# Kernel optimization log

Measured on AMD Instinct MI355X. Metric: run time of the kernel, lower is better.

Reference implementation:

```python
import jax, jax.numpy as jnp
import numpy as np
from jax import lax

NMS_TH = 0.05
TOPK_P = 1000
NMS_IOU = 0.5
NUMDETS = 100
NMS_ITERS = 15
IM = 2048.0
SIZES = [256, 128, 64, 32, 16]
NUM_CLASS = 80


def _make_boxes(key, n):
    k1, k2, k3, k4 = jax.random.split(key, 4)
    cy = jax.random.uniform(k1, (n,)) * IM
    cx = jax.random.uniform(k2, (n,)) * IM
    h = jax.random.uniform(k3, (n,)) * 300.0 + 16.0
    w = jax.random.uniform(k4, (n,)) * 300.0 + 16.0
    # yxyx boxes
    return jnp.stack([cy - h / 2, cx - w / 2, cy + h / 2, cx + w / 2], axis=1)


def setup_inputs() -> dict:
    key = jax.random.key(0)
    inp = {}
    for s, sz in enumerate(SIZES):
        kc = jax.random.fold_in(key, 2 * s)
        kb = jax.random.fold_in(key, 2 * s + 1)
        n = sz * sz
        inp['cls%d' % s] = jax.random.normal(kc, (1, n, NUM_CLASS), jnp.float32) - 2.0
        inp['reg%d' % s] = _make_boxes(kb, n)[None]
    inp['locations'] = jnp.array([0.0, 0.0, IM - 1.0, IM - 1.0, 1024.0, 1024.0], jnp.float32)
    return inp


def _pairwise_iou(a, b):
    # a: (N,4) yxyx, b: (M,4) yxyx -> (N,M)
    area_a = jnp.clip(a[:, 2] - a[:, 0], 0) * jnp.clip(a[:, 3] - a[:, 1], 0)
    area_b = jnp.clip(b[:, 2] - b[:, 0], 0) * jnp.clip(b[:, 3] - b[:, 1], 0)
    iy1 = jnp.maximum(a[:, None, 0], b[None, :, 0])
    ix1 = jnp.maximum(a[:, None, 1], b[None, :, 1])
    iy2 = jnp.minimum(a[:, None, 2], b[None, :, 2])
    ix2 = jnp.minimum(a[:, None, 3], b[None, :, 3])
    inter = jnp.clip(iy2 - iy1, 0) * jnp.clip(ix2 - ix1, 0)
    union = area_a[:, None] + area_b[None, :] - inter
    return inter / jnp.maximum(union, 1e-9)


def _cluster_nms(boxes, scores, classes, valid, iou_th):
    order = jnp.argsort(-scores)
    b = boxes[order]
    s = scores[order]
    c = classes[order]
    v = valid[order]
    iou = jnp.triu(_pairwise_iou(b, b), k=1)  # (K,K)

    def body(B, _):
        max_a = B.max(axis=0)
        keep_col = (max_a <= iou_th).astype(B.dtype)[:, None]
        return iou * keep_col, None

    B, _ = lax.scan(body, iou, None, length=NMS_ITERS)
    keep = (B.max(axis=0) <= iou_th) & v
    return b, s, c, keep


def _per_level(cls_s, reg_s):
    p = jax.nn.sigmoid(cls_s[0])                 # (N, C)
    ps = p.max(axis=1)                           # (N,)
    pi = p.argmax(axis=1).astype(jnp.int32) + 1  # class index, 0 is background
    m = ps > NMS_TH
    ps_m = jnp.where(m, ps, -1.0)
    k = min(TOPK_P, ps_m.shape[0])
    top_s, top_idx = lax.top_k(ps_m, k)
    return top_s, pi[top_idx], reg_s[0][top_idx], m[top_idx]


def reference(cls0, cls1, cls2, cls3, cls4, reg0, reg1, reg2, reg3, reg4, locations):
    levels = [(cls0, reg0), (cls1, reg1), (cls2, reg2), (cls3, reg3), (cls4, reg4)]
    sc, cl, bx, vd = [], [], [], []
    for cls_s, reg_s in levels:
        s_, c_, b_, v_ = _per_level(cls_s, reg_s)
        sc.append(s_); cl.append(c_); bx.append(b_); vd.append(v_)
    scores = jnp.concatenate(sc)
    classes = jnp.concatenate(cl)
    boxes = jnp.concatenate(bx, axis=0)
    valid = jnp.concatenate(vd)
    scores = jnp.where(valid, scores, 0.0)

    vy1, vx1, vy2, vx2 = locations[0], locations[1], locations[2], locations[3]
    ori_h, ori_w = locations[4], locations[5]
    boxes = jnp.stack([
        jnp.maximum(boxes[:, 0], vy1), jnp.maximum(boxes[:, 1], vx1),
        jnp.minimum(boxes[:, 2], vy2), jnp.minimum(boxes[:, 3], vx2)], axis=1)

    b, s, c, keep = _cluster_nms(boxes, scores, classes, valid, NMS_IOU)
    s = jnp.where(keep, s, 0.0)
    top_s, sel = lax.top_k(s, NUMDETS)
    bbox = b[sel]
    cls_out = c[sel]

    # transfer boxes back to original-image coordinates
    sy = ori_h / jnp.maximum(vy2 - vy1, 1e-6)
    sx = ori_w / jnp.maximum(vx2 - vx1, 1e-6)
    bbox = jnp.stack([
        (bbox[:, 0] - vy1) * sy, (bbox[:, 1] - vx1) * sx,
        (bbox[:, 2] - vy1) * sy, (bbox[:, 3] - vx1) * sx], axis=1)
    return bbox, cls_out, top_s
```

## Files before the change

kernel.cpp:

```cpp
#include <hip/hip_runtime.h>
#include <math.h>

#define NANCH 87296
#define NF 4256
#define CAPD 128
#define NITER 16
#define BCAP 512
#define EC 8192
#define NBLK 341
#define BASE20 0xBD4CCu
#define NB20 9216
#define BPT 9

struct InPtrs {
    const float* cls[5];
    const float* reg[5];
    const float* loc;
};

constexpr size_t SZ_HIST  = 5ull * NB20 * 4;
constexpr size_t OFF_HIST = 0;
constexpr size_t OFF_CNT  = OFF_HIST + SZ_HIST;
constexpr size_t OFF_CTR  = OFF_CNT + (size_t)NF * 4;
constexpr size_t ZERO_SZ  = OFF_CTR + 64;
constexpr size_t OFF_SBITS = ((ZERO_SZ + 255) / 256) * 256;
constexpr size_t OFF_CLSV  = OFF_SBITS + (size_t)NANCH * 4;
constexpr size_t OFF_PAR   = OFF_CLSV + (size_t)NANCH * 4;
constexpr size_t OFF_INVB  = OFF_PAR + 128;
constexpr size_t OFF_INVO  = OFF_INVB + (size_t)NBLK * 4;
constexpr size_t OFF_FINK  = ((OFF_INVO + (size_t)NBLK * 4 + 255) / 256) * 256;
constexpr size_t OFF_BBUF  = OFF_FINK + (size_t)NF * 8;
constexpr size_t OFF_SBOX  = OFF_BBUF + 5ull * BCAP * 8;
constexpr size_t OFF_SSC   = OFF_SBOX + (size_t)NF * 16;
constexpr size_t OFF_SCV   = OFF_SSC + (size_t)NF * 4;
constexpr size_t OFF_SAR   = OFF_SCV + (size_t)NF * 4;
constexpr size_t OFF_NBR   = OFF_SAR + (size_t)NF * 4;

__device__ __forceinline__ void lvl_of(int a, int& lev, int& idx) {
    if (a < 65536)      { lev = 0; idx = a; }
    else if (a < 81920) { lev = 1; idx = a - 65536; }
    else if (a < 86016) { lev = 2; idx = a - 81920; }
    else if (a < 87040) { lev = 3; idx = a - 86016; }
    else                { lev = 4; idx = a - 87040; }
}

__device__ __forceinline__ unsigned int fkey(float f) {
    unsigned int u = __float_as_uint(f);
    return u ^ ((u & 0x80000000u) ? 0xFFFFFFFFu : 0x80000000u);
}
__device__ __forceinline__ float funkey(unsigned int k) {
    return __uint_as_float(k ^ ((k & 0x80000000u) ? 0x80000000u : 0xFFFFFFFFu));
}
__device__ __forceinline__ unsigned int bin20_addr(unsigned int v) {
    unsigned int owner = v / BPT;
    unsigned int i = v - owner * BPT;
    return (i << 10) | owner;
}

__global__ __launch_bounds__(1024) void k1_score(InPtrs P, unsigned int* hist,
        unsigned int* sbits, unsigned int* clsv, unsigned int* invBlk) {
    int t = threadIdx.x;
    int a = blockIdx.x * 256 + (t >> 2);
    int k = t & 3;
    int lev, idx; lvl_of(a, lev, idx);
    const float4* row = (const float4*)(P.cls[lev] + (size_t)idx * 80);
    float4 v[5];
    #pragma unroll
    for (int q = 0; q < 5; ++q) v[q] = row[q * 4 + k];
    float best = -INFINITY; int bi = 0;
    #pragma unroll
    for (int q = 0; q < 5; ++q) {
        int c0 = q * 16 + k * 4;
        if (v[q].x > best) { best = v[q].x; bi = c0 + 0; }
        if (v[q].y > best) { best = v[q].y; bi = c0 + 1; }
        if (v[q].z > best) { best = v[q].z; bi = c0 + 2; }
        if (v[q].w > best) { best = v[q].w; bi = c0 + 3; }
    }
    #pragma unroll
    for (int m = 1; m < 4; m <<= 1) {
        float ob = __shfl_xor(best, m, 64);
        int  obi = __shfl_xor(bi, m, 64);
        if (ob > best || (ob == best && obi < bi)) { best = ob; bi = obi; }
    }
    bool lead = (k == 0);
    unsigned int valid = 0;
    if (lead) {
        float score = 1.0f / (1.0f + expf(-best));
        valid = (score > 0.05f) ? 1u : 0u;
        float psm = valid ? score : -1.0f;
        unsigned int sb = fkey(psm);
        sbits[a] = sb;
        clsv[a] = (unsigned int)(bi + 1) | (valid << 31);
        if (valid) {
            unsigned int bin = (sb >> 12) - BASE20;
            atomicAdd(&hist[(size_t)lev * NB20 + bin20_addr(bin)], 1u);
        }
    }
    __shared__ unsigned int wv[16];
    unsigned long long mv = __ballot(lead && valid);
    int lane = t & 63, w = t >> 6;
    if (lane == 0) wv[w] = (unsigned int)__popcll(mv);
    __syncthreads();
    if (t == 0) {
        unsigned int s = 0;
        #pragma unroll
        for (int i = 0; i < 16; ++i) s += wv[i];
        invBlk[blockIdx.x] = 256u - s;
    }
}

__global__ __launch_bounds__(1024) void k2_scan(const unsigned int* hist,
        const unsigned int* invBlk, unsigned int* params, unsigned int* invOff) {
    int t = threadIdx.x;
    if (blockIdx.x == 5) {
        __shared__ unsigned int sv[512];
        __shared__ unsigned int orig[512];
        if (t < 512) {
            unsigned int v = (t < NBLK) ? invBlk[t] : 0u;
            sv[t] = v; orig[t] = v;
        }
        __syncthreads();
        for (int off = 1; off < 512; off <<= 1) {
            unsigned int add = 0;
            if (t < 512 && t >= off) add = sv[t - off];
            __syncthreads();
            if (t < 512) sv[t] += add;
            __syncthreads();
        }
        if (t < NBLK) {
            int segStart = (t < 256) ? 0 : (t < 320) ? 256 : (t < 336) ? 320
                         : (t < 340) ? 336 : 340;
            invOff[t] = sv[t] - orig[t] - (segStart > 0 ? sv[segStart - 1] : 0u);
        }
        return;
    }
    int lev = blockIdx.x;
    unsigned int K = (lev == 4) ? 256u : 1000u;
    const unsigned int* h = hist + (size_t)lev * NB20;
    __shared__ unsigned int seg[1024];
    __shared__ unsigned int suf[1024];
    unsigned int hc[BPT];
    unsigned int s = 0;
    #pragma unroll
    for (int i = 0; i < BPT; ++i) { hc[i] = h[(i << 10) | t]; s += hc[i]; }
    seg[t] = s;
    suf[t] = s;
    __syncthreads();
    for (int off = 1; off < 1024; off <<= 1) {
        unsigned int v = suf[t];
        unsigned int add = (t + off < 1024) ? suf[t + off] : 0u;
        __syncthreads();
        suf[t] = v + add;
        __syncthreads();
    }
    unsigned int totValid = suf[0];
    if (totValid >= K) {
        unsigned int excl = suf[t] - seg[t];
        if (excl < K && excl + seg[t] >= K) {
            unsigned int cum = excl;
            for (int i = BPT - 1; i >= 0; --i) {
                unsigned int c = hc[i];
                if (cum + c >= K) {
                    params[lev] = (unsigned int)(t * BPT + i);
                    params[8 + lev] = K - cum;
                    params[16 + lev] = 0;
                    break;
                }
                cum += c;
            }
        }
    } else if (t == 0) {
        params[lev] = 0;
        params[8 + lev] = 0;
        params[16 + lev] = K - totValid;
    }
}

__global__ __launch_bounds__(256) void k3_compact(const unsigned int* sbits,
        const unsigned int* clsv, const unsigned int* params,
        const unsigned int* invOff, unsigned long long* finKeys,
        unsigned int* ctrs, unsigned long long* bBuf) {
    int blk = blockIdx.x;
    int t = threadIdx.x;
    int a = blk * 256 + t;
    int lev, idx; lvl_of(a, lev, idx);
    unsigned int sb = sbits[a];
    unsigned int cv = clsv[a];
    unsigned int bin = (sb >> 12) - BASE20;
    unsigned int Bs = params[lev];
    unsigned int rNeg = params[16 + lev];
    unsigned int valid = cv >> 31;
    int lane = t & 63, w = t >> 6;
    unsigned long long lt = (1ull << lane) - 1ull;
    __shared__ unsigned int wInv[4], wFin[4], wB[4];
    __shared__ unsigned int baseFin, baseB;
    unsigned long long mInv = __ballot(valid == 0u);
    if (lane == 0) wInv[w] = (unsigned int)__popcll(mInv);
    __syncthreads();
    unsigned int invRank = invOff[blk] + (unsigned int)__popcll(mInv & lt);
    for (int i = 0; i < w; ++i) invRank += wInv[i];
    bool isFin, isB;
    if (valid) {
        isFin = (bin > Bs);
        isB   = (bin == Bs);
    } else {
        isFin = (rNeg > 0) && (invRank < rNeg);
        isB   = false;
    }
    unsigned long long mFin = __ballot(isFin);
    unsigned long long mB   = __ballot(isB);
    if (lane == 0) { wFin[w] = (unsigned int)__popcll(mFin); wB[w] = (unsigned int)__popcll(mB); }
    __syncthreads();
    if (t == 0) {
        unsigned int tf = wFin[0] + wFin[1] + wFin[2] + wFin[3];
        unsigned int tb = wB[0] + wB[1] + wB[2] + wB[3];
        baseFin = tf ? atomicAdd(&ctrs[0], tf) : 0u;
        baseB   = tb ? atomicAdd(&ctrs[1 + lev], tb) : 0u;
    }
    __syncthreads();
    if (isFin || isB) {
        unsigned int composite = ((unsigned int)lev << 16) | (unsigned int)idx;
        unsigned int inv = (~composite) & 0x7FFFFu;
        unsigned int low = (inv << 13) | (valid << 7) | (cv & 0x7Fu);
        unsigned long long key = ((unsigned long long)sb << 32) | low;
        if (isFin) {
            unsigned int p = baseFin + (unsigned int)__popcll(mFin & lt);
            for (int i = 0; i < w; ++i) p += wFin[i];
            if (p < NF) finKeys[p] = key;
        } else {
            unsigned int p = baseB + (unsigned int)__popcll(mB & lt);
            for (int i = 0; i < w; ++i) p += wB[i];
            if (p < BCAP) bBuf[(size_t)lev * BCAP + p] = key;
        }
    }
}

__global__ __launch_bounds__(256) void k5_rank(InPtrs P,
        const unsigned long long* finKeys, const unsigned int* ctrs,
        const unsigned int* params, const unsigned long long* bBuf,
        float4* sBox, float* sScore, unsigned int* sCV, float* sArea) {
    __shared__ __align__(16) unsigned long long keys[NF];
    __shared__ __align__(16) unsigned long long kb[BCAP];
    __shared__ unsigned int rnk[16];
    __shared__ unsigned int posS;
    int t = threadIdx.x;
    unsigned int fc = ctrs[0];
    if (fc > NF) fc = NF;
    for (int i = t; i < (int)fc; i += 256) keys[i] = finKeys[i];
    if (t < 16) rnk[t] = 0;
    if (t == 0) posS = fc;
    __syncthreads();
    for (int lev = 0; lev < 5; ++lev) {
        unsigned int bc = ctrs[1 + lev];
        int n = (bc > BCAP) ? BCAP : (int)bc;
        int r = (int)params[8 + lev];
        if (r > n) r = n;
        if (r > 0) {
            for (int i = t; i < n; i += 256) kb[i] = bBuf[(size_t)lev * BCAP + i];
            __syncthreads();
            for (int i = t; i < n; i += 256) {
                unsigned long long my = kb[i];
                unsigned int c = 0;
                for (int j = 0; j < n; ++j) c += (kb[j] > my) ? 1u : 0u;
                if (c < (unsigned int)r) {
                    unsigned int p = atomicAdd(&posS, 1u);
                    if (p < NF) keys[p] = my;
                }
            }
            __syncthreads();
        }
    }
    unsigned int pos = posS;
    for (int i = (int)pos + t; i < NF; i += 256) keys[i] = (unsigned long long)i;
    __syncthreads();
    int lf = t & 15;
    int seg = t >> 4;
    int f = blockIdx.x * 16 + lf;
    unsigned long long my = keys[f];
    {
        unsigned int c = 0;
        const ulonglong2* kp = (const ulonglong2*)keys + seg * 133;
        #pragma unroll 4
        for (int i = 0; i < 133; ++i) {
            ulonglong2 v = kp[i];
            c += (v.x > my) ? 1u : 0u;
            c += (v.y > my) ? 1u : 0u;
        }
        atomicAdd(&rnk[lf], c);
    }
    __syncthreads();
    if (seg == 0) {
        unsigned int r = rnk[lf];
        unsigned int sb  = (unsigned int)(my >> 32);
        unsigned int low = (unsigned int)my;
        unsigned int composite = (~(low >> 13)) & 0x7FFFFu;
        int lev = composite >> 16;
        int idx = composite & 0xFFFF;
        float4 b = ((const float4*)P.reg[lev])[idx];
        float vy1 = P.loc[0], vx1 = P.loc[1], vy2 = P.loc[2], vx2 = P.loc[3];
        float y1 = fmaxf(b.x, vy1), x1 = fmaxf(b.y, vx1);
        float y2 = fminf(b.z, vy2), x2 = fminf(b.w, vx2);
        float area = __fmul_rn(fmaxf(y2 - y1, 0.0f), fmaxf(x2 - x1, 0.0f));
        unsigned int valid = (low >> 7) & 1u;
        sBox[r] = make_float4(y1, x1, y2, x2);
        sScore[r] = valid ? funkey(sb) : 0.0f;
        sCV[r] = (low & 0x7Fu) | (valid << 31);
        sArea[r] = area;
    }
}

__global__ __launch_bounds__(256) void k6_adj(const float4* sBox,
        const float* sArea, unsigned int* cnt, unsigned short* nbr) {
    int L = blockIdx.x;
    float fr = sqrtf(8.0f * (float)L + 1.0f);
    int jt = (int)((fr - 1.0f) * 0.5f);
    while ((jt + 1) * (jt + 2) / 2 <= L) jt++;
    while (jt * (jt + 1) / 2 > L) jt--;
    int it = L - jt * (jt + 1) / 2;
    __shared__ float4 cb[64]; __shared__ float ca[64];
    __shared__ float4 rb[64]; __shared__ float ra[64];
    int t = threadIdx.x;
    if (t < 64) {
        int j = jt * 64 + t;
        if (j < NF) { cb[t] = sBox[j]; ca[t] = sArea[j]; }
        int i = it * 64 + t;
        if (i < NF) { rb[t] = sBox[i]; ra[t] = sArea[i]; }
    }
    __syncthreads();
    int lj = t & 63;
    int j = jt * 64 + lj;
    if (j >= NF) return;
    float4 B = cb[lj]; float ab = ca[lj];
    for (int li = (t >> 6); li < 64; li += 4) {
        int i = it * 64 + li;
        if (i >= j) continue;
        float4 A = rb[li]; float aa = ra[li];
        float iy1 = fmaxf(A.x, B.x), ix1 = fmaxf(A.y, B.y);
        float iy2 = fminf(A.z, B.z), ix2 = fminf(A.w, B.w);
        float ih = fmaxf(iy2 - iy1, 0.0f), iw = fmaxf(ix2 - ix1, 0.0f);
        float inter = __fmul_rn(ih, iw);
        float uni = __fsub_rn(__fadd_rn(aa, ab), inter);
        float iou = __fdiv_rn(inter, fmaxf(uni, 1e-9f));
        if (iou > 0.5f) {
            unsigned int p = atomicAdd(&cnt[j], 1u);
            if (p < CAPD) nbr[(size_t)j * CAPD + p] = (unsigned short)i;
        }
    }
}

__global__ __launch_bounds__(1024) void k7_nms(InPtrs P, const float4* sBox,
        const float* sScore, const unsigned int* sCV, const unsigned int* cnt,
        const unsigned short* nbr, float* out) {
    __shared__ unsigned int edges[EC];
    __shared__ __align__(4) unsigned char bufA[NF];
    __shared__ __align__(4) unsigned char bufB[NF];
    __shared__ unsigned int wsum[16];
    __shared__ float ploc[6];
    int t = threadIdx.x;
    int lane = t & 63, wid = t >> 6;
    if (t < 6) ploc[t] = P.loc[t];
    const int CH = 5;
    unsigned int dq[CH];
    unsigned int s = 0;
    #pragma unroll
    for (int q = 0; q < CH; ++q) {
        int j = t * CH + q;
        unsigned int d = 0;
        if (j < NF) { d = cnt[j]; if (d > CAPD) d = CAPD; }
        dq[q] = d; s += d;
    }
    unsigned int sc = s;
    #pragma unroll
    for (int o = 1; o < 64; o <<= 1) {
        unsigned int n = __shfl_up(sc, o, 64);
        if (lane >= o) sc += n;
    }
    if (lane == 63) wsum[wid] = sc;
    if (t < 1064) ((unsigned int*)bufA)[t] = 0x01010101u;
    __syncthreads();
    unsigned int wbase = 0, tot = 0;
    #pragma unroll
    for (int i = 0; i < 16; ++i) {
        unsigned int v = wsum[i];
        if (i < wid) wbase += v;
        tot += v;
    }
    unsigned int E = tot;
    bool useLds = (E <= (unsigned int)EC);
    if (useLds) {
        unsigned int base = wbase + sc - s;
        #pragma unroll
        for (int q = 0; q < CH; ++q) {
            int j = t * CH + q;
            if (j < NF) {
                unsigned int d = dq[q];
                const unsigned short* nl = nbr + (size_t)j * CAPD;
                for (unsigned int e = 0; e < d; ++e)
                    edges[base + e] = ((unsigned int)nl[e] << 16) | (unsigned int)j;
                base += d;
            }
        }
    }
    __syncthreads();
    unsigned char* cur = bufA; unsigned char* nxt = bufB;
    if (useLds) {
        for (int itr = 0; itr < NITER; ++itr) {
            if (t < 1064) ((unsigned int*)nxt)[t] = 0x01010101u;
            __syncthreads();
            for (int e = t; e < (int)E; e += 1024) {
                unsigned int pk = edges[e];
                if (cur[pk >> 16]) nxt[pk & 0xFFFFu] = 0;
            }
            __syncthreads();
            unsigned char* tm = cur; cur = nxt; nxt = tm;
        }
    } else {
        for (int itr = 0; itr < NITER; ++itr) {
            for (int j = t; j < NF; j += 1024) {
                unsigned int d = cnt[j]; if (d > CAPD) d = CAPD;
                const unsigned short* nl = nbr + (size_t)j * CAPD;
                unsigned char kp = 1;
                for (unsigned int e = 0; e < d; ++e)
                    if (cur[nl[e]]) { kp = 0; break; }
                nxt[j] = kp;
            }
            __syncthreads();
            unsigned char* tm = cur; cur = nxt; nxt = tm;
        }
    }
    int base = t * CH;
    unsigned char kf[CH];
    unsigned int sum = 0;
    #pragma unroll
    for (int q = 0; q < CH; ++q) {
        int j = base + q;
        unsigned char v = 0;
        if (j < NF) v = cur[j] & (unsigned char)(sCV[j] >> 31);
        kf[q] = v; sum += v;
    }
    unsigned int sc2 = sum;
    #pragma unroll
    for (int o = 1; o < 64; o <<= 1) {
        unsigned int n = __shfl_up(sc2, o, 64);
        if (lane >= o) sc2 += n;
    }
    if (lane == 63) wsum[wid] = sc2;
    __syncthreads();
    unsigned int wbase2 = 0, keptTot = 0;
    #pragma unroll
    for (int i = 0; i < 16; ++i) {
        unsigned int v = wsum[i];
        if (i < wid) wbase2 += v;
        keptTot += v;
    }
    unsigned int run = wbase2 + sc2 - sum;
    float vy1 = ploc[0], vx1 = ploc[1], vy2 = ploc[2], vx2 = ploc[3];
    float sy = ploc[4] / fmaxf(vy2 - vy1, 1e-6f);
    float sx = ploc[5] / fmaxf(vx2 - vx1, 1e-6f);
    #pragma unroll
    for (int q = 0; q < CH; ++q) {
        int j = base + q;
        if (j >= NF) break;
        unsigned int slot = 0xFFFFFFFFu;
        float scv = 0.0f;
        if (kf[q]) {
            if (run < 100u) { slot = run; scv = sScore[j]; }
            run++;
        } else if (keptTot < 100u) {
            unsigned int nk = (unsigned int)j - run;
            unsigned int s2 = keptTot + nk;
            if (s2 < 100u) { slot = s2; scv = 0.0f; }
        }
        if (slot < 100u) {
            float4 b = sBox[j];
            out[slot * 4 + 0] = (b.x - vy1) * sy;
            out[slot * 4 + 1] = (b.y - vx1) * sx;
            out[slot * 4 + 2] = (b.z - vy1) * sy;
            out[slot * 4 + 3] = (b.w - vx1) * sx;
            out[400 + slot] = (float)(sCV[j] & 0x7Fu);
            out[500 + slot] = scv;
        }
    }
}

extern "C" void kernel_launch(void* const* d_in, const int* in_sizes, int n_in,
                              void* d_out, int out_size, void* d_ws, size_t ws_size,
                              hipStream_t stream) {
    (void)n_in; (void)out_size; (void)ws_size;
    InPtrs P;
    bool inter = (in_sizes[1] == 65536 * 4);
    for (int s = 0; s < 5; ++s) {
        P.cls[s] = (const float*)d_in[inter ? 2 * s : s];
        P.reg[s] = (const float*)d_in[inter ? 2 * s + 1 : 5 + s];
    }
    P.loc = (const float*)d_in[10];

    char* w = (char*)d_ws;
    unsigned int* hist   = (unsigned int*)(w + OFF_HIST);
    unsigned int* cnt    = (unsigned int*)(w + OFF_CNT);
    unsigned int* ctrs   = (unsigned int*)(w + OFF_CTR);
    unsigned int* sbits  = (unsigned int*)(w + OFF_SBITS);
    unsigned int* clsv   = (unsigned int*)(w + OFF_CLSV);
    unsigned int* params = (unsigned int*)(w + OFF_PAR);
    unsigned int* invBlk = (unsigned int*)(w + OFF_INVB);
    unsigned int* invOff = (unsigned int*)(w + OFF_INVO);
    unsigned long long* finKeys = (unsigned long long*)(w + OFF_FINK);
    unsigned long long* bBuf    = (unsigned long long*)(w + OFF_BBUF);
    float4* sBox  = (float4*)(w + OFF_SBOX);
    float* sScore = (float*)(w + OFF_SSC);
    unsigned int* sCV = (unsigned int*)(w + OFF_SCV);
    float* sArea  = (float*)(w + OFF_SAR);
    unsigned short* nbr = (unsigned short*)(w + OFF_NBR);

    hipMemsetAsync(d_ws, 0, ZERO_SZ, stream);
    k1_score<<<NBLK, 1024, 0, stream>>>(P, hist, sbits, clsv, invBlk);
    k2_scan<<<6, 1024, 0, stream>>>(hist, invBlk, params, invOff);
    k3_compact<<<NBLK, 256, 0, stream>>>(sbits, clsv, params, invOff, finKeys, ctrs, bBuf);
    k5_rank<<<266, 256, 0, stream>>>(P, finKeys, ctrs, params, bBuf, sBox, sScore, sCV, sArea);
    k6_adj<<<2278, 256, 0, stream>>>(sBox, sArea, cnt, nbr);
    k7_nms<<<1, 1024, 0, stream>>>(P, sBox, sScore, sCV, cnt, nbr, (float*)d_out);
}
```

Before: 174.6 us.

## Fuse all pipeline stages into one persistent kernel with grid barriers

Replaces six separate kernel launches with a single persistent kernel of 192 blocks that runs each stage in a grid-stride or subset-of-blocks loop, separated by atomic-counter grid barriers. Shared memory is reused through a union across stages, and the barrier counters are zeroed by the existing memset, which is enlarged to cover them. The aim is to remove per-launch overhead and inter-kernel gaps. In exchange, many stages now run on fewer blocks, and the spin barriers rely on all 192 blocks being co-resident.

```diff
diff --git a/kernel.cpp b/kernel.cpp
--- a/kernel.cpp
+++ b/kernel.cpp
@@ -1,5 +1,6 @@
 #include <hip/hip_runtime.h>
 #include <math.h>
+
 
 #define NANCH 87296
 #define NF 4256
@@ -11,6 +12,8 @@
 #define BASE20 0xBD4CCu
 #define NB20 9216
 #define BPT 9
+#define NBLOCKS 192
+#define NTILE 2278
 
 struct InPtrs {
     const float* cls[5];
@@ -22,7 +25,7 @@
 constexpr size_t OFF_HIST = 0;
 constexpr size_t OFF_CNT  = OFF_HIST + SZ_HIST;
 constexpr size_t OFF_CTR  = OFF_CNT + (size_t)NF * 4;
-constexpr size_t ZERO_SZ  = OFF_CTR + 64;
+constexpr size_t ZERO_SZ  = OFF_CTR + 1024;
 constexpr size_t OFF_SBITS = ((ZERO_SZ + 255) / 256) * 256;
 constexpr size_t OFF_CLSV  = OFF_SBITS + (size_t)NANCH * 4;
 constexpr size_t OFF_PAR   = OFF_CLSV + (size_t)NANCH * 4;
@@ -57,428 +60,475 @@
     return (i << 10) | owner;
 }
 
-__global__ __launch_bounds__(1024) void k1_score(InPtrs P, unsigned int* hist,
-        unsigned int* sbits, unsigned int* clsv, unsigned int* invBlk) {
-    int t = threadIdx.x;
-    int a = blockIdx.x * 256 + (t >> 2);
-    int k = t & 3;
-    int lev, idx; lvl_of(a, lev, idx);
-    const float4* row = (const float4*)(P.cls[lev] + (size_t)idx * 80);
-    float4 v[5];
-    #pragma unroll
-    for (int q = 0; q < 5; ++q) v[q] = row[q * 4 + k];
-    float best = -INFINITY; int bi = 0;
-    #pragma unroll
-    for (int q = 0; q < 5; ++q) {
-        int c0 = q * 16 + k * 4;
-        if (v[q].x > best) { best = v[q].x; bi = c0 + 0; }
-        if (v[q].y > best) { best = v[q].y; bi = c0 + 1; }
-        if (v[q].z > best) { best = v[q].z; bi = c0 + 2; }
-        if (v[q].w > best) { best = v[q].w; bi = c0 + 3; }
-    }
-    #pragma unroll
-    for (int m = 1; m < 4; m <<= 1) {
-        float ob = __shfl_xor(best, m, 64);
-        int  obi = __shfl_xor(bi, m, 64);
-        if (ob > best || (ob == best && obi < bi)) { best = ob; bi = obi; }
-    }
-    bool lead = (k == 0);
-    unsigned int valid = 0;
-    if (lead) {
-        float score = 1.0f / (1.0f + expf(-best));
-        valid = (score > 0.05f) ? 1u : 0u;
-        float psm = valid ? score : -1.0f;
-        unsigned int sb = fkey(psm);
-        sbits[a] = sb;
-        clsv[a] = (unsigned int)(bi + 1) | (valid << 31);
-        if (valid) {
-            unsigned int bin = (sb >> 12) - BASE20;
-            atomicAdd(&hist[(size_t)lev * NB20 + bin20_addr(bin)], 1u);
-        }
-    }
-    __shared__ unsigned int wv[16];
-    unsigned long long mv = __ballot(lead && valid);
-    int lane = t & 63, w = t >> 6;
-    if (lane == 0) wv[w] = (unsigned int)__popcll(mv);
+__device__ __forceinline__ void gbar(unsigned int* c) {
     __syncthreads();
-    if (t == 0) {
+    if (threadIdx.x == 0) {
+        __threadfence();
+        atomicAdd(c, 1u);
+        while (__hip_atomic_load(c, __ATOMIC_RELAXED, __HIP_MEMORY_SCOPE_AGENT)
+               < (unsigned int)NBLOCKS)
+            __builtin_amdgcn_s_sleep(8);
+        __threadfence();
+    }
+    __syncthreads();
+}
+
+union SMem {
+    struct { unsigned int wv[16]; } p1;
+    struct { unsigned int sv[512]; unsigned int orig[512]; } p2i;
+    struct { unsigned int seg[1024]; unsigned int suf[1024]; } p2;
+    struct { unsigned int wInv[16], wFin[16], wB[16];
+             unsigned int baseFin[4], baseB[4]; } p3;
+    struct { unsigned long long keys[NF]; unsigned long long kb[BCAP];
+             unsigned int rnk[64]; unsigned int posS; } p4;
+    struct { float4 cb[4][64]; float ca[4][64];
+             float4 rb[4][64]; float ra[4][64]; } p5;
+    struct { unsigned int edges[EC]; unsigned char bufA[NF];
+             unsigned char bufB[NF]; unsigned int wsum[16];
+             float ploc[6]; } p6;
+};
+
+__global__ __launch_bounds__(1024, 4) void fused_all(InPtrs P, char* __restrict__ ws,
+                                                     float* __restrict__ out) {
+    __shared__ __align__(16) SMem sm;
+    const int t = threadIdx.x;
+
+    unsigned int* hist   = (unsigned int*)(ws + OFF_HIST);
+    unsigned int* cnt    = (unsigned int*)(ws + OFF_CNT);
+    unsigned int* ctrs   = (unsigned int*)(ws + OFF_CTR);
+    unsigned int* bar    = ctrs + 32;
+    unsigned int* sbits  = (unsigned int*)(ws + OFF_SBITS);
+    unsigned int* clsv   = (unsigned int*)(ws + OFF_CLSV);
+    unsigned int* params = (unsigned int*)(ws + OFF_PAR);
+    unsigned int* invBlk = (unsigned int*)(ws + OFF_INVB);
+    unsigned int* invOff = (unsigned int*)(ws + OFF_INVO);
+    unsigned long long* finKeys = (unsigned long long*)(ws + OFF_FINK);
+    unsigned long long* bBuf    = (unsigned long long*)(ws + OFF_BBUF);
+    float4* sBox  = (float4*)(ws + OFF_SBOX);
+    float* sScore = (float*)(ws + OFF_SSC);
+    unsigned int* sCV = (unsigned int*)(ws + OFF_SCV);
+    float* sArea  = (float*)(ws + OFF_SAR);
+    unsigned short* nbr = (unsigned short*)(ws + OFF_NBR);
+
+    for (int vb = blockIdx.x; vb < NBLK; vb += NBLOCKS) {
+        __syncthreads();
+        int a = vb * 256 + (t >> 2);
+        int k = t & 3;
+        int lev, idx; lvl_of(a, lev, idx);
+        const float4* row = (const float4*)(P.cls[lev] + (size_t)idx * 80);
+        float4 v[5];
+        #pragma unroll
+        for (int q = 0; q < 5; ++q) v[q] = row[q * 4 + k];
+        float best = -INFINITY; int bi = 0;
+        #pragma unroll
+        for (int q = 0; q < 5; ++q) {
+            int c0 = q * 16 + k * 4;
+            if (v[q].x > best) { best = v[q].x; bi = c0 + 0; }
+            if (v[q].y > best) { best = v[q].y; bi = c0 + 1; }
+            if (v[q].z > best) { best = v[q].z; bi = c0 + 2; }
+            if (v[q].w > best) { best = v[q].w; bi = c0 + 3; }
+        }
+        #pragma unroll
+        for (int m = 1; m < 4; m <<= 1) {
+            float ob = __shfl_xor(best, m, 64);
+            int  obi = __shfl_xor(bi, m, 64);
+            if (ob > best || (ob == best && obi < bi)) { best = ob; bi = obi; }
+        }
+        bool lead = (k == 0);
+        unsigned int valid = 0;
+        if (lead) {
+            float score = 1.0f / (1.0f + expf(-best));
+            valid = (score > 0.05f) ? 1u : 0u;
+            float psm = valid ? score : -1.0f;
+            unsigned int sb = fkey(psm);
+            sbits[a] = sb;
+            clsv[a] = (unsigned int)(bi + 1) | (valid << 31);
+            if (valid) {
+                unsigned int bin = (sb >> 12) - BASE20;
+                atomicAdd(&hist[(size_t)lev * NB20 + bin20_addr(bin)], 1u);
+            }
+        }
+        unsigned long long mv = __ballot(lead && valid);
+        int lane = t & 63, w = t >> 6;
+        if (lane == 0) sm.p1.wv[w] = (unsigned int)__popcll(mv);
+        __syncthreads();
+        if (t == 0) {
+            unsigned int s = 0;
+            #pragma unroll
+            for (int i = 0; i < 16; ++i) s += sm.p1.wv[i];
+            invBlk[vb] = 256u - s;
+        }
+    }
+    gbar(bar + 0 * 32);
+
+    if (blockIdx.x < 6) {
+        if (blockIdx.x == 5) {
+            if (t < 512) {
+                unsigned int v = (t < NBLK) ? invBlk[t] : 0u;
+                sm.p2i.sv[t] = v; sm.p2i.orig[t] = v;
+            }
+            __syncthreads();
+            for (int off = 1; off < 512; off <<= 1) {
+                unsigned int add = 0;
+                if (t < 512 && t >= off) add = sm.p2i.sv[t - off];
+                __syncthreads();
+                if (t < 512) sm.p2i.sv[t] += add;
+                __syncthreads();
+            }
+            if (t < NBLK) {
+                int segStart = (t < 256) ? 0 : (t < 320) ? 256 : (t < 336) ? 320
+                             : (t < 340) ? 336 : 340;
+                invOff[t] = sm.p2i.sv[t] - sm.p2i.orig[t]
+                          - (segStart > 0 ? sm.p2i.sv[segStart - 1] : 0u);
+            }
+        } else {
+            int lev = blockIdx.x;
+            unsigned int K = (lev == 4) ? 256u : 1000u;
+            const unsigned int* h = hist + (size_t)lev * NB20;
+            unsigned int hc[BPT];
+            unsigned int s = 0;
+            #pragma unroll
+            for (int i = 0; i < BPT; ++i) { hc[i] = h[(i << 10) | t]; s += hc[i]; }
+            sm.p2.seg[t] = s;
+            sm.p2.suf[t] = s;
+            __syncthreads();
+            for (int off = 1; off < 1024; off <<= 1) {
+                unsigned int v = sm.p2.suf[t];
+                unsigned int add = (t + off < 1024) ? sm.p2.suf[t + off] : 0u;
+                __syncthreads();
+                sm.p2.suf[t] = v + add;
+                __syncthreads();
+            }
+            unsigned int totValid = sm.p2.suf[0];
+            if (totValid >= K) {
+                unsigned int excl = sm.p2.suf[t] - sm.p2.seg[t];
+                if (excl < K && excl + sm.p2.seg[t] >= K) {
+                    unsigned int cum = excl;
+                    for (int i = BPT - 1; i >= 0; --i) {
+                        unsigned int c = hc[i];
+                        if (cum + c >= K) {
+                            params[lev] = (unsigned int)(t * BPT + i);
+                            params[8 + lev] = K - cum;
+                            params[16 + lev] = 0;
+                            break;
+                        }
+                        cum += c;
+                    }
+                }
+            } else if (t == 0) {
+                params[lev] = 0;
+                params[8 + lev] = 0;
+                params[16 + lev] = K - totValid;
+            }
+        }
+    }
+    gbar(bar + 1 * 32);
+
+    if (blockIdx.x < 86) {
+        int sub = t >> 8, tt = t & 255;
+        int vb = blockIdx.x * 4 + sub;
+        bool act = (vb < NBLK);
+        int a = act ? vb * 256 + tt : 0;
+        int lev, idx; lvl_of(a, lev, idx);
+        unsigned int sb = 0u, cv = 0u;
+        if (act) { sb = sbits[a]; cv = clsv[a]; }
+        unsigned int bin = (sb >> 12) - BASE20;
+        unsigned int Bs = params[lev];
+        unsigned int rNeg = params[16 + lev];
+        unsigned int valid = cv >> 31;
+        int lane = t & 63;
+        int w16 = t >> 6, wl = w16 & 3;
+        unsigned long long lt = (1ull << lane) - 1ull;
+        unsigned long long mInv = __ballot(act && valid == 0u);
+        if (lane == 0) sm.p3.wInv[w16] = (unsigned int)__popcll(mInv);
+        __syncthreads();
+        unsigned int invRank = (act ? invOff[vb] : 0u) + (unsigned int)__popcll(mInv & lt);
+        for (int i = 0; i < wl; ++i) invRank += sm.p3.wInv[sub * 4 + i];
+        bool isFin = false, isB = false;
+        if (act) {
+            if (valid) { isFin = (bin > Bs); isB = (bin == Bs); }
+            else       { isFin = (rNeg > 0) && (invRank < rNeg); }
+        }
+        unsigned long long mFin = __ballot(isFin);
+        unsigned long long mB   = __ballot(isB);
+        if (lane == 0) {
+            sm.p3.wFin[w16] = (unsigned int)__popcll(mFin);
+            sm.p3.wB[w16]   = (unsigned int)__popcll(mB);
+        }
+        __syncthreads();
+        if (tt == 0) {
+            unsigned int tf = 0, tb = 0;
+            #pragma unroll
+            for (int i = 0; i < 4; ++i) {
+                tf += sm.p3.wFin[sub * 4 + i];
+                tb += sm.p3.wB[sub * 4 + i];
+            }
+            sm.p3.baseFin[sub] = tf ? atomicAdd(&ctrs[0], tf) : 0u;
+            sm.p3.baseB[sub]   = tb ? atomicAdd(&ctrs[1 + lev], tb) : 0u;
+        }
+        __syncthreads();
+        if (isFin || isB) {
+            unsigned int composite = ((unsigned int)lev << 16) | (unsigned int)idx;
+            unsigned int inv = (~composite) & 0x7FFFFu;
+            unsigned int low = (inv << 13) | (valid << 7) | (cv & 0x7Fu);
+            unsigned long long key = ((unsigned long long)sb << 32) | low;
+            if (isFin) {
+                unsigned int p = sm.p3.baseFin[sub] + (unsigned int)__popcll(mFin & lt);
+                for (int i = 0; i < wl; ++i) p += sm.p3.wFin[sub * 4 + i];
+                if (p < NF) finKeys[p] = key;
+            } else {
+                unsigned int p = sm.p3.baseB[sub] + (unsigned int)__popcll(mB & lt);
+                for (int i = 0; i < wl; ++i) p += sm.p3.wB[sub * 4 + i];
+                if (p < BCAP) bBuf[(size_t)lev * BCAP + p] = key;
+            }
+        }
+    }
+    gbar(bar + 2 * 32);
+
+    if (blockIdx.x < 67) {
+        unsigned int fc = ctrs[0];
+        if (fc > NF) fc = NF;
+        for (int i = t; i < (int)fc; i += 1024) sm.p4.keys[i] = finKeys[i];
+        if (t < 64) sm.p4.rnk[t] = 0;
+        if (t == 0) sm.p4.posS = fc;
+        __syncthreads();
+        for (int lev = 0; lev < 5; ++lev) {
+            unsigned int bc = ctrs[1 + lev];
+            int n = (bc > BCAP) ? BCAP : (int)bc;
+            int r = (int)params[8 + lev];
+            if (r > n) r = n;
+            if (r > 0) {
+                for (int i = t; i < n; i += 1024) sm.p4.kb[i] = bBuf[(size_t)lev * BCAP + i];
+                __syncthreads();
+                for (int i = t; i < n; i += 1024) {
+                    unsigned long long my = sm.p4.kb[i];
+                    unsigned int c = 0;
+                    for (int j = 0; j < n; ++j) c += (sm.p4.kb[j] > my) ? 1u : 0u;
+                    if (c < (unsigned int)r) {
+                        unsigned int p = atomicAdd(&sm.p4.posS, 1u);
+                        if (p < NF) sm.p4.keys[p] = my;
+                    }
+                }
+                __syncthreads();
+            }
+        }
+        unsigned int pos = sm.p4.posS;
+        for (int i = (int)pos + t; i < NF; i += 1024) sm.p4.keys[i] = (unsigned long long)i;
+        __syncthreads();
+        int lf = t & 63;
+        int seg = t >> 6;
+        int f = blockIdx.x * 64 + lf;
+        unsigned long long my = (f < NF) ? sm.p4.keys[f] : 0ull;
+        {
+            unsigned int c = 0;
+            const ulonglong2* kp = (const ulonglong2*)sm.p4.keys + seg * 133;
+            #pragma unroll 4
+            for (int i = 0; i < 133; ++i) {
+                ulonglong2 v2 = kp[i];
+                c += (v2.x > my) ? 1u : 0u;
+                c += (v2.y > my) ? 1u : 0u;
+            }
+            if (f < NF) atomicAdd(&sm.p4.rnk[lf], c);
+        }
+        __syncthreads();
+        if (seg == 0 && f < NF) {
+            unsigned int r = sm.p4.rnk[lf];
+            unsigned int sbv = (unsigned int)(my >> 32);
+            unsigned int low = (unsigned int)my;
+            unsigned int composite = (~(low >> 13)) & 0x7FFFFu;
+            int lev = composite >> 16;
+            int idx = composite & 0xFFFF;
+            float4 b = ((const float4*)P.reg[lev])[idx];
+            float vy1 = P.loc[0], vx1 = P.loc[1], vy2 = P.loc[2], vx2 = P.loc[3];
+            float y1 = fmaxf(b.x, vy1), x1 = fmaxf(b.y, vx1);
+            float y2 = fminf(b.z, vy2), x2 = fminf(b.w, vx2);
+            float area = __fmul_rn(fmaxf(y2 - y1, 0.0f), fmaxf(x2 - x1, 0.0f));
+            unsigned int valid = (low >> 7) & 1u;
+            sBox[r] = make_float4(y1, x1, y2, x2);
+            sScore[r] = valid ? funkey(sbv) : 0.0f;
+            sCV[r] = (low & 0x7Fu) | (valid << 31);
+            sArea[r] = area;
+        }
+    }
+    gbar(bar + 3 * 32);
+
+    {
+        int sub = t >> 8, tt = t & 255;
+        for (int rep = 0; rep < 3; ++rep) {
+            int vb = rep * (NBLOCKS * 4) + blockIdx.x * 4 + sub;
+            __syncthreads();
+            bool act = (vb < NTILE);
+            int jt = 0, ii = 0;
+            if (act) {
+                float fr = sqrtf(8.0f * (float)vb + 1.0f);
+                jt = (int)((fr - 1.0f) * 0.5f);
+                while ((jt + 1) * (jt + 2) / 2 <= vb) jt++;
+                while (jt * (jt + 1) / 2 > vb) jt--;
+                ii = vb - jt * (jt + 1) / 2;
+                if (tt < 64) {
+                    int j = jt * 64 + tt;
+                    if (j < NF) { sm.p5.cb[sub][tt] = sBox[j]; sm.p5.ca[sub][tt] = sArea[j]; }
+                    int i = ii * 64 + tt;
+                    if (i < NF) { sm.p5.rb[sub][tt] = sBox[i]; sm.p5.ra[sub][tt] = sArea[i]; }
+                }
+            }
+            __syncthreads();
+            if (act) {
+                int lj = tt & 63;
+                int j = jt * 64 + lj;
+                if (j < NF) {
+                    float4 B = sm.p5.cb[sub][lj]; float ab = sm.p5.ca[sub][lj];
+                    for (int li = (tt >> 6); li < 64; li += 4) {
+                        int i = ii * 64 + li;
+                        if (i >= j) continue;
+                        float4 A = sm.p5.rb[sub][li]; float aa = sm.p5.ra[sub][li];
+                        float iy1 = fmaxf(A.x, B.x), ix1 = fmaxf(A.y, B.y);
+                        float iy2 = fminf(A.z, B.z), ix2 = fminf(A.w, B.w);
+                        float ih = fmaxf(iy2 - iy1, 0.0f), iw = fmaxf(ix2 - ix1, 0.0f);
+                        float inter = __fmul_rn(ih, iw);
+                        float uni = __fsub_rn(__fadd_rn(aa, ab), inter);
+                        float iou = __fdiv_rn(inter, fmaxf(uni, 1e-9f));
+                        if (iou > 0.5f) {
+                            unsigned int p = atomicAdd(&cnt[j], 1u);
+                            if (p < CAPD) nbr[(size_t)j * CAPD + p] = (unsigned short)i;
+                        }
+                    }
+                }
+            }
+        }
+    }
+    gbar(bar + 4 * 32);
+
+    if (blockIdx.x != 0) return;
+    {
+        unsigned int* edges = sm.p6.edges;
+        unsigned char* bufA = sm.p6.bufA;
+        unsigned char* bufB = sm.p6.bufB;
+        unsigned int* wsum = sm.p6.wsum;
+        float* ploc = sm.p6.ploc;
+        int lane = t & 63, wid = t >> 6;
+        if (t < 6) ploc[t] = P.loc[t];
+        const int CH = 5;
+        unsigned int dq[CH];
         unsigned int s = 0;
-        #pragma unroll
-        for (int i = 0; i < 16; ++i) s += wv[i];
-        invBlk[blockIdx.x] = 256u - s;
-    }
-}
-
-__global__ __launch_bounds__(1024) void k2_scan(const unsigned int* hist,
-        const unsigned int* invBlk, unsigned int* params, unsigned int* invOff) {
-    int t = threadIdx.x;
-    if (blockIdx.x == 5) {
-        __shared__ unsigned int sv[512];
-        __shared__ unsigned int orig[512];
-        if (t < 512) {
-            unsigned int v = (t < NBLK) ? invBlk[t] : 0u;
-            sv[t] = v; orig[t] = v;
-        }
-        __syncthreads();
-        for (int off = 1; off < 512; off <<= 1) {
-            unsigned int add = 0;
-            if (t < 512 && t >= off) add = sv[t - off];
-            __syncthreads();
-            if (t < 512) sv[t] += add;
-            __syncthreads();
-        }
-        if (t < NBLK) {
-            int segStart = (t < 256) ? 0 : (t < 320) ? 256 : (t < 336) ? 320
-                         : (t < 340) ? 336 : 340;
-            invOff[t] = sv[t] - orig[t] - (segStart > 0 ? sv[segStart - 1] : 0u);
-        }
-        return;
-    }
-    int lev = blockIdx.x;
-    unsigned int K = (lev == 4) ? 256u : 1000u;
-    const unsigned int* h = hist + (size_t)lev * NB20;
-    __shared__ unsigned int seg[1024];
-    __shared__ unsigned int suf[1024];
-    unsigned int hc[BPT];
-    unsigned int s = 0;
-    #pragma unroll
-    for (int i = 0; i < BPT; ++i) { hc[i] = h[(i << 10) | t]; s += hc[i]; }
-    seg[t] = s;
-    suf[t] = s;
-    __syncthreads();
-    for (int off = 1; off < 1024; off <<= 1) {
-        unsigned int v = suf[t];
-        unsigned int add = (t + off < 1024) ? suf[t + off] : 0u;
-        __syncthreads();
-        suf[t] = v + add;
-        __syncthreads();
-    }
-    unsigned int totValid = suf[0];
-    if (totValid >= K) {
-        unsigned int excl = suf[t] - seg[t];
-        if (excl < K && excl + seg[t] >= K) {
-            unsigned int cum = excl;
-            for (int i = BPT - 1; i >= 0; --i) {
-                unsigned int c = hc[i];
-                if (cum + c >= K) {
-                    params[lev] = (unsigned int)(t * BPT + i);
-                    params[8 + lev] = K - cum;
-                    params[16 + lev] = 0;
-                    break;
-                }
-                cum += c;
-            }
-        }
-    } else if (t == 0) {
-        params[lev] = 0;
-        params[8 + lev] = 0;
-        params[16 + lev] = K - totValid;
-    }
-}
-
-__global__ __launch_bounds__(256) void k3_compact(const unsigned int* sbits,
-        const unsigned int* clsv, const unsigned int* params,
-        const unsigned int* invOff, unsigned long long* finKeys,
-        unsigned int* ctrs, unsigned long long* bBuf) {
-    int blk = blockIdx.x;
-    int t = threadIdx.x;
-    int a = blk * 256 + t;
-    int lev, idx; lvl_of(a, lev, idx);
-    unsigned int sb = sbits[a];
-    unsigned int cv = clsv[a];
-    unsigned int bin = (sb >> 12) - BASE20;
-    unsigned int Bs = params[lev];
-    unsigned int rNeg = params[16 + lev];
-    unsigned int valid = cv >> 31;
-    int lane = t & 63, w = t >> 6;
-    unsigned long long lt = (1ull << lane) - 1ull;
-    __shared__ unsigned int wInv[4], wFin[4], wB[4];
-    __shared__ unsigned int baseFin, baseB;
-    unsigned long long mInv = __ballot(valid == 0u);
-    if (lane == 0) wInv[w] = (unsigned int)__popcll(mInv);
-    __syncthreads();
-    unsigned int invRank = invOff[blk] + (unsigned int)__popcll(mInv & lt);
-    for (int i = 0; i < w; ++i) invRank += wInv[i];
-    bool isFin, isB;
-    if (valid) {
-        isFin = (bin > Bs);
-        isB   = (bin == Bs);
-    } else {
-        isFin = (rNeg > 0) && (invRank < rNeg);
-        isB   = false;
-    }
-    unsigned long long mFin = __ballot(isFin);
-    unsigned long long mB   = __ballot(isB);
-    if (lane == 0) { wFin[w] = (unsigned int)__popcll(mFin); wB[w] = (unsigned int)__popcll(mB); }
-    __syncthreads();
-    if (t == 0) {
-        unsigned int tf = wFin[0] + wFin[1] + wFin[2] + wFin[3];
-        unsigned int tb = wB[0] + wB[1] + wB[2] + wB[3];
-        baseFin = tf ? atomicAdd(&ctrs[0], tf) : 0u;
-        baseB   = tb ? atomicAdd(&ctrs[1 + lev], tb) : 0u;
-    }
-    __syncthreads();
-    if (isFin || isB) {
-        unsigned int composite = ((unsigned int)lev << 16) | (unsigned int)idx;
-        unsigned int inv = (~composite) & 0x7FFFFu;
-        unsigned int low = (inv << 13) | (valid << 7) | (cv & 0x7Fu);
-        unsigned long long key = ((unsigned long long)sb << 32) | low;
-        if (isFin) {
-            unsigned int p = baseFin + (unsigned int)__popcll(mFin & lt);
-            for (int i = 0; i < w; ++i) p += wFin[i];
-            if (p < NF) finKeys[p] = key;
-        } else {
-            unsigned int p = baseB + (unsigned int)__popcll(mB & lt);
-            for (int i = 0; i < w; ++i) p += wB[i];
-            if (p < BCAP) bBuf[(size_t)lev * BCAP + p] = key;
-        }
-    }
-}
-
-__global__ __launch_bounds__(256) void k5_rank(InPtrs P,
-        const unsigned long long* finKeys, const unsigned int* ctrs,
-        const unsigned int* params, const unsigned long long* bBuf,
-        float4* sBox, float* sScore, unsigned int* sCV, float* sArea) {
-    __shared__ __align__(16) unsigned long long keys[NF];
-    __shared__ __align__(16) unsigned long long kb[BCAP];
-    __shared__ unsigned int rnk[16];
-    __shared__ unsigned int posS;
-    int t = threadIdx.x;
-    unsigned int fc = ctrs[0];
-    if (fc > NF) fc = NF;
-    for (int i = t; i < (int)fc; i += 256) keys[i] = finKeys[i];
-    if (t < 16) rnk[t] = 0;
-    if (t == 0) posS = fc;
-    __syncthreads();
-    for (int lev = 0; lev < 5; ++lev) {
-        unsigned int bc = ctrs[1 + lev];
-        int n = (bc > BCAP) ? BCAP : (int)bc;
-        int r = (int)params[8 + lev];
-        if (r > n) r = n;
-        if (r > 0) {
-            for (int i = t; i < n; i += 256) kb[i] = bBuf[(size_t)lev * BCAP + i];
-            __syncthreads();
-            for (int i = t; i < n; i += 256) {
-                unsigned long long my = kb[i];
-                unsigned int c = 0;
-                for (int j = 0; j < n; ++j) c += (kb[j] > my) ? 1u : 0u;
-                if (c < (unsigned int)r) {
-                    unsigned int p = atomicAdd(&posS, 1u);
-                    if (p < NF) keys[p] = my;
-                }
-            }
-            __syncthreads();
-        }
-    }
-    unsigned int pos = posS;
-    for (int i = (int)pos + t; i < NF; i += 256) keys[i] = (unsigned long long)i;
-    __syncthreads();
-    int lf = t & 15;
-    int seg = t >> 4;
-    int f = blockIdx.x * 16 + lf;
-    unsigned long long my = keys[f];
-    {
-        unsigned int c = 0;
-        const ulonglong2* kp = (const ulonglong2*)keys + seg * 133;
-        #pragma unroll 4
-        for (int i = 0; i < 133; ++i) {
-            ulonglong2 v = kp[i];
-            c += (v.x > my) ? 1u : 0u;
-            c += (v.y > my) ? 1u : 0u;
-        }
-        atomicAdd(&rnk[lf], c);
-    }
-    __syncthreads();
-    if (seg == 0) {
-        unsigned int r = rnk[lf];
-        unsigned int sb  = (unsigned int)(my >> 32);
-        unsigned int low = (unsigned int)my;
-        unsigned int composite = (~(low >> 13)) & 0x7FFFFu;
-        int lev = composite >> 16;
-        int idx = composite & 0xFFFF;
-        float4 b = ((const float4*)P.reg[lev])[idx];
-        float vy1 = P.loc[0], vx1 = P.loc[1], vy2 = P.loc[2], vx2 = P.loc[3];
-        float y1 = fmaxf(b.x, vy1), x1 = fmaxf(b.y, vx1);
-        float y2 = fminf(b.z, vy2), x2 = fminf(b.w, vx2);
-        float area = __fmul_rn(fmaxf(y2 - y1, 0.0f), fmaxf(x2 - x1, 0.0f));
-        unsigned int valid = (low >> 7) & 1u;
-        sBox[r] = make_float4(y1, x1, y2, x2);
-        sScore[r] = valid ? funkey(sb) : 0.0f;
-        sCV[r] = (low & 0x7Fu) | (valid << 31);
-        sArea[r] = area;
-    }
-}
-
-__global__ __launch_bounds__(256) void k6_adj(const float4* sBox,
-        const float* sArea, unsigned int* cnt, unsigned short* nbr) {
-    int L = blockIdx.x;
-    float fr = sqrtf(8.0f * (float)L + 1.0f);
-    int jt = (int)((fr - 1.0f) * 0.5f);
-    while ((jt + 1) * (jt + 2) / 2 <= L) jt++;
-    while (jt * (jt + 1) / 2 > L) jt--;
-    int it = L - jt * (jt + 1) / 2;
-    __shared__ float4 cb[64]; __shared__ float ca[64];
-    __shared__ float4 rb[64]; __shared__ float ra[64];
-    int t = threadIdx.x;
-    if (t < 64) {
-        int j = jt * 64 + t;
-        if (j < NF) { cb[t] = sBox[j]; ca[t] = sArea[j]; }
-        int i = it * 64 + t;
-        if (i < NF) { rb[t] = sBox[i]; ra[t] = sArea[i]; }
-    }
-    __syncthreads();
-    int lj = t & 63;
-    int j = jt * 64 + lj;
-    if (j >= NF) return;
-    float4 B = cb[lj]; float ab = ca[lj];
-    for (int li = (t >> 6); li < 64; li += 4) {
-        int i = it * 64 + li;
-        if (i >= j) continue;
-        float4 A = rb[li]; float aa = ra[li];
-        float iy1 = fmaxf(A.x, B.x), ix1 = fmaxf(A.y, B.y);
-        float iy2 = fminf(A.z, B.z), ix2 = fminf(A.w, B.w);
-        float ih = fmaxf(iy2 - iy1, 0.0f), iw = fmaxf(ix2 - ix1, 0.0f);
-        float inter = __fmul_rn(ih, iw);
-        float uni = __fsub_rn(__fadd_rn(aa, ab), inter);
-        float iou = __fdiv_rn(inter, fmaxf(uni, 1e-9f));
-        if (iou > 0.5f) {
-            unsigned int p = atomicAdd(&cnt[j], 1u);
-            if (p < CAPD) nbr[(size_t)j * CAPD + p] = (unsigned short)i;
-        }
-    }
-}
-
-__global__ __launch_bounds__(1024) void k7_nms(InPtrs P, const float4* sBox,
-        const float* sScore, const unsigned int* sCV, const unsigned int* cnt,
-        const unsigned short* nbr, float* out) {
-    __shared__ unsigned int edges[EC];
-    __shared__ __align__(4) unsigned char bufA[NF];
-    __shared__ __align__(4) unsigned char bufB[NF];
-    __shared__ unsigned int wsum[16];
-    __shared__ float ploc[6];
-    int t = threadIdx.x;
-    int lane = t & 63, wid = t >> 6;
-    if (t < 6) ploc[t] = P.loc[t];
-    const int CH = 5;
-    unsigned int dq[CH];
-    unsigned int s = 0;
-    #pragma unroll
-    for (int q = 0; q < CH; ++q) {
-        int j = t * CH + q;
-        unsigned int d = 0;
-        if (j < NF) { d = cnt[j]; if (d > CAPD) d = CAPD; }
-        dq[q] = d; s += d;
-    }
-    unsigned int sc = s;
-    #pragma unroll
-    for (int o = 1; o < 64; o <<= 1) {
-        unsigned int n = __shfl_up(sc, o, 64);
-        if (lane >= o) sc += n;
-    }
-    if (lane == 63) wsum[wid] = sc;
-    if (t < 1064) ((unsigned int*)bufA)[t] = 0x01010101u;
-    __syncthreads();
-    unsigned int wbase = 0, tot = 0;
-    #pragma unroll
-    for (int i = 0; i < 16; ++i) {
-        unsigned int v = wsum[i];
-        if (i < wid) wbase += v;
-        tot += v;
-    }
-    unsigned int E = tot;
-    bool useLds = (E <= (unsigned int)EC);
-    if (useLds) {
-        unsigned int base = wbase + sc - s;
         #pragma unroll
         for (int q = 0; q < CH; ++q) {
             int j = t * CH + q;
-            if (j < NF) {
-                unsigned int d = dq[q];
-                const unsigned short* nl = nbr + (size_t)j * CAPD;
-                for (unsigned int e = 0; e < d; ++e)
-                    edges[base + e] = ((unsigned int)nl[e] << 16) | (unsigned int)j;
-                base += d;
-            }
-        }
-    }
-    __syncthreads();
-    unsigned char* cur = bufA; unsigned char* nxt = bufB;
-    if (useLds) {
-        for (int itr = 0; itr < NITER; ++itr) {
-            if (t < 1064) ((unsigned int*)nxt)[t] = 0x01010101u;
-            __syncthreads();
-            for (int e = t; e < (int)E; e += 1024) {
-                unsigned int pk = edges[e];
-                if (cur[pk >> 16]) nxt[pk & 0xFFFFu] = 0;
-            }
-            __syncthreads();
-            unsigned char* tm = cur; cur = nxt; nxt = tm;
-        }
-    } else {
-        for (int itr = 0; itr < NITER; ++itr) {
-            for (int j = t; j < NF; j += 1024) {
-                unsigned int d = cnt[j]; if (d > CAPD) d = CAPD;
-                const unsigned short* nl = nbr + (size_t)j * CAPD;
-                unsigned char kp = 1;
-                for (unsigned int e = 0; e < d; ++e)
-                    if (cur[nl[e]]) { kp = 0; break; }
-                nxt[j] = kp;
-            }
-            __syncthreads();
-            unsigned char* tm = cur; cur = nxt; nxt = tm;
-        }
-    }
-    int base = t * CH;
-    unsigned char kf[CH];
-    unsigned int sum = 0;
-    #pragma unroll
-    for (int q = 0; q < CH; ++q) {
-        int j = base + q;
-        unsigned char v = 0;
-        if (j < NF) v = cur[j] & (unsigned char)(sCV[j] >> 31);
-        kf[q] = v; sum += v;
-    }
-    unsigned int sc2 = sum;
-    #pragma unroll
-    for (int o = 1; o < 64; o <<= 1) {
-        unsigned int n = __shfl_up(sc2, o, 64);
-        if (lane >= o) sc2 += n;
-    }
-    if (lane == 63) wsum[wid] = sc2;
-    __syncthreads();
-    unsigned int wbase2 = 0, keptTot = 0;
-    #pragma unroll
-    for (int i = 0; i < 16; ++i) {
-        unsigned int v = wsum[i];
-        if (i < wid) wbase2 += v;
-        keptTot += v;
-    }
-    unsigned int run = wbase2 + sc2 - sum;
-    float vy1 = ploc[0], vx1 = ploc[1], vy2 = ploc[2], vx2 = ploc[3];
-    float sy = ploc[4] / fmaxf(vy2 - vy1, 1e-6f);
-    float sx = ploc[5] / fmaxf(vx2 - vx1, 1e-6f);
-    #pragma unroll
-    for (int q = 0; q < CH; ++q) {
-        int j = base + q;
-        if (j >= NF) break;
-        unsigned int slot = 0xFFFFFFFFu;
-        float scv = 0.0f;
-        if (kf[q]) {
-            if (run < 100u) { slot = run; scv = sScore[j]; }
-            run++;
-        } else if (keptTot < 100u) {
-            unsigned int nk = (unsigned int)j - run;
-            unsigned int s2 = keptTot + nk;
-            if (s2 < 100u) { slot = s2; scv = 0.0f; }
-        }
-        if (slot < 100u) {
-            float4 b = sBox[j];
-            out[slot * 4 + 0] = (b.x - vy1) * sy;
-            out[slot * 4 + 1] = (b.y - vx1) * sx;
-            out[slot * 4 + 2] = (b.z - vy1) * sy;
-            out[slot * 4 + 3] = (b.w - vx1) * sx;
-            out[400 + slot] = (float)(sCV[j] & 0x7Fu);
-            out[500 + slot] = scv;
+            unsigned int d = 0;
+            if (j < NF) { d = cnt[j]; if (d > CAPD) d = CAPD; }
+            dq[q] = d; s += d;
+        }
+        unsigned int sc = s;
+        #pragma unroll
+        for (int o = 1; o < 64; o <<= 1) {
+            unsigned int n = __shfl_up(sc, o, 64);
+            if (lane >= o) sc += n;
+        }
+        if (lane == 63) wsum[wid] = sc;
+        if (t < 1064) ((unsigned int*)bufA)[t] = 0x01010101u;
+        __syncthreads();
+        unsigned int wbase = 0, tot = 0;
+        #pragma unroll
+        for (int i = 0; i < 16; ++i) {
+            unsigned int v = wsum[i];
+            if (i < wid) wbase += v;
+            tot += v;
+        }
+        unsigned int E = tot;
+        bool useLds = (E <= (unsigned int)EC);
+        if (useLds) {
+            unsigned int base = wbase + sc - s;
+            #pragma unroll
+            for (int q = 0; q < CH; ++q) {
+                int j = t * CH + q;
+                if (j < NF) {
+                    unsigned int d = dq[q];
+                    const unsigned short* nl = nbr + (size_t)j * CAPD;
+                    for (unsigned int e = 0; e < d; ++e)
+                        edges[base + e] = ((unsigned int)nl[e] << 16) | (unsigned int)j;
+                    base += d;
+                }
+            }
+        }
+        __syncthreads();
+        unsigned char* cur = bufA; unsigned char* nxt = bufB;
+        if (useLds) {
+            for (int itr = 0; itr < NITER; ++itr) {
+                if (t < 1064) ((unsigned int*)nxt)[t] = 0x01010101u;
+                __syncthreads();
+                for (int e = t; e < (int)E; e += 1024) {
+                    unsigned int pk = edges[e];
+                    if (cur[pk >> 16]) nxt[pk & 0xFFFFu] = 0;
+                }
+                __syncthreads();
+                unsigned char* tm = cur; cur = nxt; nxt = tm;
+            }
+        } else {
+            for (int itr = 0; itr < NITER; ++itr) {
+                for (int j = t; j < NF; j += 1024) {
+                    unsigned int d = cnt[j]; if (d > CAPD) d = CAPD;
+                    const unsigned short* nl = nbr + (size_t)j * CAPD;
+                    unsigned char kp = 1;
+                    for (unsigned int e = 0; e < d; ++e)
+                        if (cur[nl[e]]) { kp = 0; break; }
+                    nxt[j] = kp;
+                }
+                __syncthreads();
+                unsigned char* tm = cur; cur = nxt; nxt = tm;
+            }
+        }
+        int base = t * CH;
+        unsigned char kf[CH];
+        unsigned int sum = 0;
+        #pragma unroll
+        for (int q = 0; q < CH; ++q) {
+            int j = base + q;
+            unsigned char v = 0;
+            if (j < NF) v = cur[j] & (unsigned char)(sCV[j] >> 31);
+            kf[q] = v; sum += v;
+        }
+        unsigned int sc2 = sum;
+        #pragma unroll
+        for (int o = 1; o < 64; o <<= 1) {
+            unsigned int n = __shfl_up(sc2, o, 64);
+            if (lane >= o) sc2 += n;
+        }
+        if (lane == 63) wsum[wid] = sc2;
+        __syncthreads();
+        unsigned int wbase2 = 0, keptTot = 0;
+        #pragma unroll
+        for (int i = 0; i < 16; ++i) {
+            unsigned int v = wsum[i];
+            if (i < wid) wbase2 += v;
+            keptTot += v;
+        }
+        unsigned int run = wbase2 + sc2 - sum;
+        float vy1 = ploc[0], vx1 = ploc[1], vy2 = ploc[2], vx2 = ploc[3];
+        float sy = ploc[4] / fmaxf(vy2 - vy1, 1e-6f);
+        float sx = ploc[5] / fmaxf(vx2 - vx1, 1e-6f);
+        #pragma unroll
+        for (int q = 0; q < CH; ++q) {
+            int j = base + q;
+            if (j >= NF) break;
+            unsigned int slot = 0xFFFFFFFFu;
+            float scv = 0.0f;
+            if (kf[q]) {
+                if (run < 100u) { slot = run; scv = sScore[j]; }
+                run++;
+            } else if (keptTot < 100u) {
+                unsigned int nk = (unsigned int)j - run;
+                unsigned int s2 = keptTot + nk;
+                if (s2 < 100u) { slot = s2; scv = 0.0f; }
+            }
+            if (slot < 100u) {
+                float4 b = sBox[j];
+                out[slot * 4 + 0] = (b.x - vy1) * sy;
+                out[slot * 4 + 1] = (b.y - vx1) * sx;
+                out[slot * 4 + 2] = (b.z - vy1) * sy;
+                out[slot * 4 + 3] = (b.w - vx1) * sx;
+                out[400 + slot] = (float)(sCV[j] & 0x7Fu);
+                out[500 + slot] = scv;
+            }
         }
     }
 }
@@ -495,28 +545,6 @@
     }
     P.loc = (const float*)d_in[10];
 
-    char* w = (char*)d_ws;
-    unsigned int* hist   = (unsigned int*)(w + OFF_HIST);
-    unsigned int* cnt    = (unsigned int*)(w + OFF_CNT);
-    unsigned int* ctrs   = (unsigned int*)(w + OFF_CTR);
-    unsigned int* sbits  = (unsigned int*)(w + OFF_SBITS);
-    unsigned int* clsv   = (unsigned int*)(w + OFF_CLSV);
-    unsigned int* params = (unsigned int*)(w + OFF_PAR);
-    unsigned int* invBlk = (unsigned int*)(w + OFF_INVB);
-    unsigned int* invOff = (unsigned int*)(w + OFF_INVO);
-    unsigned long long* finKeys = (unsigned long long*)(w + OFF_FINK);
-    unsigned long long* bBuf    = (unsigned long long*)(w + OFF_BBUF);
-    float4* sBox  = (float4*)(w + OFF_SBOX);
-    float* sScore = (float*)(w + OFF_SSC);
-    unsigned int* sCV = (unsigned int*)(w + OFF_SCV);
-    float* sArea  = (float*)(w + OFF_SAR);
-    unsigned short* nbr = (unsigned short*)(w + OFF_NBR);
-
     hipMemsetAsync(d_ws, 0, ZERO_SZ, stream);
-    k1_score<<<NBLK, 1024, 0, stream>>>(P, hist, sbits, clsv, invBlk);
-    k2_scan<<<6, 1024, 0, stream>>>(hist, invBlk, params, invOff);
-    k3_compact<<<NBLK, 256, 0, stream>>>(sbits, clsv, params, invOff, finKeys, ctrs, bBuf);
-    k5_rank<<<266, 256, 0, stream>>>(P, finKeys, ctrs, params, bBuf, sBox, sScore, sCV, sArea);
-    k6_adj<<<2278, 256, 0, stream>>>(sBox, sArea, cnt, nbr);
-    k7_nms<<<1, 1024, 0, stream>>>(P, sBox, sScore, sCV, cnt, nbr, (float*)d_out);
-}
+    fused_all<<<NBLOCKS, 1024, 0, stream>>>(P, (char*)d_ws, (float*)d_out);
+}
```

Result: slower. 225.3 us (+29.0%).
